# Kernel tuning notes

Measured on AMD Instinct MI355X. Metric: run time of the kernel, lower is better.

## Reference

```python
import jax, jax.numpy as jnp
import numpy as np

LN_EPS = 1e-5  # torch F.layer_norm default

def _layer_norm(c):
    mu = jnp.mean(c, axis=-1, keepdims=True)
    var = jnp.mean((c - mu) ** 2, axis=-1, keepdims=True)
    return (c - mu) * jax.lax.rsqrt(var + LN_EPS)

def _ln_lstm_cell(x, h, c, wx, wh, b):
    # wx: (4, H, in)  used as x @ wx[g].T ; wh: (4, H, H) used as h @ wh[g] (NO transpose,
    # matching the original torch code which only transposes the input weight).
    # gate order: i, f, o, c_tilde
    pre = jnp.einsum('bi,ghi->gbh', x, wx) + jnp.einsum('bh,ghk->gbk', h, wh) + b[:, None, :]
    i = jax.nn.sigmoid(pre[0])
    f = jax.nn.sigmoid(pre[1])
    o = jax.nn.sigmoid(pre[2])
    c_tilde = jnp.tanh(pre[3])
    c_new = _layer_norm(f * c + i * c_tilde)
    h_new = o * jnp.tanh(c_new)
    return h_new, c_new

def setup_inputs() -> dict:
    key = jax.random.key(0)
    ks = jax.random.split(key, 8)
    BS, SEQ, OBS, H, LOGIT = 512, 64, 512, 1024, 1024
    w = lambda k, *s: jax.random.normal(k, s, jnp.float32) * 0.02
    return {
        'obs': jax.random.normal(ks[0], (BS, SEQ, OBS), jnp.float32),
        'fc1_w': w(ks[1], H, OBS),
        'fc1_b': jnp.zeros((H,), jnp.float32),
        'wx1': w(ks[2], 4, H, H),
        'wh1': w(ks[3], 4, H, H),
        'b1': jnp.zeros((4, H), jnp.float32),
        'wx2': w(ks[4], 4, H, H),
        'wh2': w(ks[5], 4, H, H),
        'b2': jnp.zeros((4, H), jnp.float32),
        'fc2_w': w(ks[6], LOGIT, H),
        'fc2_b': jnp.zeros((LOGIT,), jnp.float32),
    }

def reference(obs, fc1_w, fc1_b, wx1, wh1, b1, wx2, wh2, b2, fc2_w, fc2_b):
    # obs: (bs, seq, obs_shape)
    x = jnp.einsum('bso,ho->bsh', obs, fc1_w) + fc1_b  # fc1 over all timesteps
    bs, seq, H = x.shape
    z = jnp.zeros((bs, H), x.dtype)

    def step(carry, xt):
        h0, c0, h1, c1 = carry
        h0, c0 = _ln_lstm_cell(xt, h0, c0, wx1, wh1, b1)  # layer 1
        h1, c1 = _ln_lstm_cell(h0, h1, c1, wx2, wh2, b2)  # layer 2 (dropout = identity in eval)
        return (h0, c0, h1, c1), None

    (h0, c0, h1, c1), _ = jax.lax.scan(step, (z, z, z, z), jnp.swapaxes(x, 0, 1))
    logit = h1 @ fc2_w.T + fc2_b
    h_n = jnp.stack((h0, h1), axis=0)
    c_n = jnp.stack((c0, c1), axis=0)
    return logit, h_n, c_n
```

## Files before the change

### kernel.cpp

```cpp
#include <hip/hip_runtime.h>
#include <hip/hip_bf16.h>
#include <hip/hip_fp16.h>

using half_t = _Float16;
typedef __attribute__((ext_vector_type(8))) _Float16 f16x8;
typedef __attribute__((ext_vector_type(4))) _Float16 f16x4;
typedef __attribute__((ext_vector_type(4))) float f32x4;

#define LN_EPS 1e-5f

__device__ inline void gll16(const void* g, void* ldsbase) {
    __builtin_amdgcn_global_load_lds(
        (const __attribute__((address_space(1))) void*)g,
        (__attribute__((address_space(3))) void*)ldsbase, 16, 0, 0);
}

__device__ inline float block_sum(float v, float* sred) {
    #pragma unroll
    for (int off = 32; off; off >>= 1) v += __shfl_down(v, off, 64);
    __syncthreads();
    if ((threadIdx.x & 63) == 0) sred[threadIdx.x >> 6] = v;
    __syncthreads();
    return sred[0] + sred[1] + sred[2] + sred[3];
}

__device__ inline void cell_block(
    int b, const half_t* __restrict__ preA, const half_t* __restrict__ preB,
    const float* __restrict__ bias,
    float* __restrict__ cst, half_t* __restrict__ hs,
    float* __restrict__ hf, bool final_step)
{
    __shared__ float sred[4];
    const int t = threadIdx.x;
    const int hi = t * 4;
    const size_t pb = (size_t)b * 4096 + hi;
    const size_t cb = (size_t)b * 1024 + hi;

    float pre[4][4];
    #pragma unroll
    for (int g = 0; g < 4; ++g) {
        f16x4 a4 = *(const f16x4*)&preA[pb + g*1024];
        f16x4 v4 = *(const f16x4*)&preB[pb + g*1024];
        float4 bs = *(const float4*)&bias[g*1024 + hi];
        pre[g][0] = (float)a4[0] + (float)v4[0] + bs.x;
        pre[g][1] = (float)a4[1] + (float)v4[1] + bs.y;
        pre[g][2] = (float)a4[2] + (float)v4[2] + bs.z;
        pre[g][3] = (float)a4[3] + (float)v4[3] + bs.w;
    }
    float4 c4 = *(const float4*)&cst[cb];
    float co[4] = {c4.x, c4.y, c4.z, c4.w};

    float cn[4], og[4], s = 0.f;
    #pragma unroll
    for (int j = 0; j < 4; ++j) {
        float ig = 1.f / (1.f + expf(-pre[0][j]));
        float fg = 1.f / (1.f + expf(-pre[1][j]));
        og[j]    = 1.f / (1.f + expf(-pre[2][j]));
        float ct = tanhf(pre[3][j]);
        cn[j] = fg * co[j] + ig * ct;
        s += cn[j];
    }
    float mu  = block_sum(s, sred) * (1.f/1024.f);
    float vs = 0.f;
    #pragma unroll
    for (int j = 0; j < 4; ++j) { float d = cn[j] - mu; vs += d*d; }
    float var = block_sum(vs, sred) * (1.f/1024.f);
    float rs  = rsqrtf(var + LN_EPS);

    float4 cw, hw; f16x4 h16w;
    #pragma unroll
    for (int j = 0; j < 4; ++j) {
        float cv = (cn[j] - mu) * rs;
        float hv = og[j] * tanhf(cv);
        ((float*)&cw)[j] = cv;
        ((float*)&hw)[j] = hv;
        h16w[j] = (half_t)hv;
    }
    *(float4*)&cst[cb] = cw;
    *(f16x4*)&hs[cb]   = h16w;
    if (final_step) *(float4*)&hf[cb] = hw;
}

__global__ __launch_bounds__(256) void cells_kernel(
    const half_t* __restrict__ preA1_rd, const half_t* __restrict__ preB1,
    const half_t* __restrict__ preA2,    const half_t* __restrict__ preB2,
    const float* __restrict__ b1, const float* __restrict__ b2,
    float* __restrict__ c0, float* __restrict__ c1,
    half_t* __restrict__ h0s, half_t* __restrict__ h1s,
    float* __restrict__ h0f, float* __restrict__ h1f, int st)
{
    const int blk = blockIdx.x;
    if (blk < 512) {
        cell_block(blk, preA1_rd, preB1, b1, c0, h0s, h0f, st == 63);
    } else {
        if (st == 0) return;
        cell_block(blk - 512, preA2, preB2, b2, c1, h1s, h1f, false);
    }
}

__global__ __launch_bounds__(256) void cells_final(
    const half_t* __restrict__ preA2, const half_t* __restrict__ preB2,
    const float* __restrict__ b2,
    float* __restrict__ c1, half_t* __restrict__ h1s, float* __restrict__ h1f)
{
    cell_block(blockIdx.x, preA2, preB2, b2, c1, h1s, h1f, true);
}

__global__ __launch_bounds__(256, 2) void step_gemm4(
    const half_t* __restrict__ X,
    const half_t* __restrict__ wx1c, const half_t* __restrict__ wx2c,
    const half_t* __restrict__ wh1t, const half_t* __restrict__ wh2t,
    half_t* __restrict__ preA1_wr, half_t* __restrict__ preA2,
    half_t* __restrict__ preB1, half_t* __restrict__ preB2,
    const half_t* __restrict__ h0s, const half_t* __restrict__ h1s, int st)
{
    __shared__ __align__(16) unsigned char sA[2][16384];
    __shared__ __align__(16) unsigned char sB[2][16384];

    const int wg = blockIdx.x;
    const int ylo = wg & 7;
    int r = wg >> 3;
    const int x = r & 3; r >>= 2;
    const int z = r & 3; r >>= 2;
    const int y = ylo + 8 * r;

    if (z == 3 && st == 63) return;

    const half_t* A; const half_t* B; half_t* C; size_t lda;
    if (z == 0)      { A = h0s; lda = 1024; B = wx2c; C = preA2; }
    else if (z == 1) { A = h1s; lda = 1024; B = wh2t; C = preB2; }
    else if (z == 2) { A = h0s; lda = 1024; B = wh1t; C = preB1; }
    else { A = X + (size_t)(st+1) * 1024; lda = 65536; B = wx1c; C = preA1_wr; }

    const int t = threadIdx.x, l = t & 63, w = t >> 6;
    const int wr = (w >> 1) * 64, wc = (w & 1) * 64;
    const int rowbase = x * 128, colbase = y * 128;

    int srow[4], sch[4];
    #pragma unroll
    for (int i = 0; i < 4; ++i) {
        int s = (w*4 + i)*64 + l;
        srow[i] = s >> 3;
        sch[i]  = ((s & 7) ^ (srow[i] & 7)) * 8;
    }

    f32x4 acc[4][4];
    #pragma unroll
    for (int m = 0; m < 4; ++m)
        #pragma unroll
        for (int n = 0; n < 4; ++n) acc[m][n] = (f32x4)(0.f);

    auto stage = [&](int kt, int buf) {
        const int ko = kt * 64;
        #pragma unroll
        for (int i = 0; i < 4; ++i) {
            gll16(A + (size_t)(rowbase+srow[i])*lda + ko + sch[i], &sA[buf][(w*4+i)*1024]);
            gll16(B + (size_t)(colbase+srow[i])*1024 + ko + sch[i], &sB[buf][(w*4+i)*1024]);
        }
    };

    stage(0, 0);
    for (int kt = 0; kt < 16; ++kt) {
        const int buf = kt & 1;
        __syncthreads();
        if (kt + 1 < 16) stage(kt + 1, buf ^ 1);
        #pragma unroll
        for (int kk = 0; kk < 2; ++kk) {
            const int chunk = kk*4 + (l >> 4);
            f16x8 bfr[4];
            #pragma unroll
            for (int n = 0; n < 4; ++n) {
                int rowb = wc + n*16 + (l & 15);
                bfr[n] = *(const f16x8*)&sB[buf][rowb*128 + ((chunk ^ (rowb & 7)) << 4)];
            }
            #pragma unroll
            for (int m = 0; m < 4; ++m) {
                int rowa = wr + m*16 + (l & 15);
                f16x8 af = *(const f16x8*)&sA[buf][rowa*128 + ((chunk ^ (rowa & 7)) << 4)];
                #pragma unroll
                for (int n = 0; n < 4; ++n)
                    acc[m][n] = __builtin_amdgcn_mfma_f32_16x16x32_f16(af, bfr[n], acc[m][n], 0, 0, 0);
            }
        }
    }

    #pragma unroll
    for (int m = 0; m < 4; ++m) {
        int row0 = rowbase + wr + m*16 + (l >> 4)*4;
        #pragma unroll
        for (int n = 0; n < 4; ++n) {
            int col = colbase + wc + n*16 + (l & 15);
            #pragma unroll
            for (int r2 = 0; r2 < 4; ++r2)
                C[(size_t)(row0+r2)*4096 + col] = (half_t)acc[m][n][r2];
        }
    }
}

struct GArgs {
    const half_t* A; const half_t* B; const float* bias; void* C;
    int lda, ldb, K, ldc, outhalf;
};

__global__ __launch_bounds__(256) void gemm_ms(GArgs g0, GArgs g1, GArgs g2,
                                               int gx, int gy, int gz, int rowpin)
{
    const int d = blockIdx.x;
    int x, y, z;
    if (rowpin) {
        const int xlo = d & 7;
        int r = d >> 3;
        y = r % gy;  r /= gy;
        z = r % gz;
        x = xlo + 8 * (r / gz);
    } else {
        const int ylo = d & 7;
        int r = d >> 3;
        x = r % gx;  r /= gx;
        z = r % gz;
        y = ylo + 8 * (r / gz);
    }

    const GArgs g = (z == 0) ? g0 : (z == 1 ? g1 : g2);

    __shared__ __align__(16) unsigned char sA[2][16384];
    __shared__ __align__(16) unsigned char sB[2][16384];

    const int t  = threadIdx.x;
    const int l  = t & 63;
    const int w  = t >> 6;
    const int wr = (w >> 1) * 64;
    const int wc = (w & 1)  * 64;
    const int rowbase = x * 128;
    const int colbase = y * 128;

    f32x4 acc[4][4];
    #pragma unroll
    for (int m = 0; m < 4; ++m)
        #pragma unroll
        for (int n = 0; n < 4; ++n) acc[m][n] = (f32x4)(0.f);

    int srow[4], sch[4];
    #pragma unroll
    for (int i = 0; i < 4; ++i) {
        int s = (w*4 + i)*64 + l;
        srow[i] = s >> 3;
        sch[i]  = ((s & 7) ^ (srow[i] & 7)) * 8;
    }

    const int nkt = g.K >> 6;

    auto stage = [&](int kt, int buf) {
        const int ko = kt * 64;
        #pragma unroll
        for (int i = 0; i < 4; ++i) {
            gll16(g.A + (size_t)(rowbase+srow[i])*g.lda + ko + sch[i], &sA[buf][(w*4+i)*1024]);
            gll16(g.B + (size_t)(colbase+srow[i])*g.ldb + ko + sch[i], &sB[buf][(w*4+i)*1024]);
        }
    };

    stage(0, 0);
    for (int kt = 0; kt < nkt; ++kt) {
        const int buf = kt & 1;
        __syncthreads();
        if (kt + 1 < nkt) stage(kt + 1, buf ^ 1);
        #pragma unroll
        for (int kk = 0; kk < 2; ++kk) {
            const int chunk = kk*4 + (l >> 4);
            f16x8 bfr[4];
            #pragma unroll
            for (int n = 0; n < 4; ++n) {
                int rowb = wc + n*16 + (l & 15);
                bfr[n] = *(const f16x8*)&sB[buf][rowb*128 + ((chunk ^ (rowb & 7)) << 4)];
            }
            #pragma unroll
            for (int m = 0; m < 4; ++m) {
                int rowa = wr + m*16 + (l & 15);
                f16x8 af = *(const f16x8*)&sA[buf][rowa*128 + ((chunk ^ (rowa & 7)) << 4)];
                #pragma unroll
                for (int n = 0; n < 4; ++n)
                    acc[m][n] = __builtin_amdgcn_mfma_f32_16x16x32_f16(af, bfr[n], acc[m][n], 0, 0, 0);
            }
        }
    }

    #pragma unroll
    for (int m = 0; m < 4; ++m) {
        int row0 = rowbase + wr + m*16 + (l >> 4)*4;
        #pragma unroll
        for (int n = 0; n < 4; ++n) {
            int col = colbase + wc + n*16 + (l & 15);
            float bv = g.bias ? g.bias[col] : 0.f;
            #pragma unroll
            for (int r2 = 0; r2 < 4; ++r2) {
                float v = acc[m][n][r2] + bv;
                if (g.outhalf) ((half_t*)g.C)[(size_t)(row0+r2)*g.ldc + col] = (half_t)v;
                else           ((float*)g.C)[(size_t)(row0+r2)*g.ldc + col] = v;
            }
        }
    }
}

__global__ __launch_bounds__(256) void transpose_wh_cvt(
    const float* __restrict__ wh1, const float* __restrict__ wh2,
    half_t* __restrict__ o1, half_t* __restrict__ o2)
{
    __shared__ float tile[64][65];
    const int z = blockIdx.z;
    const float* src = (z < 4 ? wh1 : wh2) + (size_t)(z & 3) * 1024 * 1024;
    half_t*      dst = (z < 4 ? o1  : o2 ) + (size_t)(z & 3) * 1024 * 1024;
    const int kb = blockIdx.x * 64, nb = blockIdx.y * 64;
    const int t = threadIdx.x;
    #pragma unroll
    for (int i = 0; i < 16; ++i) {
        int idx = t + i*256, r = idx >> 6, c = idx & 63;
        tile[r][c] = src[(size_t)(kb + r)*1024 + nb + c];
    }
    __syncthreads();
    #pragma unroll
    for (int i = 0; i < 16; ++i) {
        int idx = t + i*256, r = idx >> 6, c = idx & 63;
        dst[(size_t)(nb + r)*1024 + kb + c] = (half_t)tile[c][r];
    }
}

__global__ __launch_bounds__(256) void cvt_f32_f16(
    const float* __restrict__ in, half_t* __restrict__ out, int n8)
{
    int i = blockIdx.x * 256 + threadIdx.x;
    if (i >= n8) return;
    float4 lo = ((const float4*)in)[2*i];
    float4 hi = ((const float4*)in)[2*i + 1];
    union { uint4 v; half_t h[8]; } r;
    r.h[0]=(half_t)lo.x; r.h[1]=(half_t)lo.y; r.h[2]=(half_t)lo.z; r.h[3]=(half_t)lo.w;
    r.h[4]=(half_t)hi.x; r.h[5]=(half_t)hi.y; r.h[6]=(half_t)hi.z; r.h[7]=(half_t)hi.w;
    ((uint4*)out)[i] = r.v;
}

__global__ __launch_bounds__(256) void pack_out(
    const float* __restrict__ h0, const float* __restrict__ h1,
    const float* __restrict__ c0, const float* __restrict__ c1, float* __restrict__ out)
{
    const int NSZ = 512 * 1024;
    int i = blockIdx.x * 256 + threadIdx.x;
    out[NSZ     + i] = h0[i];
    out[2*NSZ   + i] = h1[i];
    out[3*NSZ   + i] = c0[i];
    out[4*NSZ   + i] = c1[i];
}

extern "C" void kernel_launch(void* const* d_in, const int* in_sizes, int n_in,
                              void* d_out, int out_size, void* d_ws, size_t ws_size,
                              hipStream_t stream)
{
    const float* obs   = (const float*)d_in[0];
    const float* fc1_w = (const float*)d_in[1];
    const float* fc1_b = (const float*)d_in[2];
    const float* wx1   = (const float*)d_in[3];
    const float* wh1   = (const float*)d_in[4];
    const float* b1    = (const float*)d_in[5];
    const float* wx2   = (const float*)d_in[6];
    const float* wh2   = (const float*)d_in[7];
    const float* b2    = (const float*)d_in[8];
    const float* fc2_w = (const float*)d_in[9];
    const float* fc2_b = (const float*)d_in[10];
    float* out = (float*)d_out;

    char* ws = (char*)d_ws;
    size_t off = 0;
    auto carve = [&](size_t bytes) -> char* {
        char* p = ws + off; off += (bytes + 255) & ~(size_t)255; return p;
    };
    half_t* obs16 = (half_t*)carve((size_t)512*64*512*2);
    half_t* wx1c  = (half_t*)carve((size_t)4096*1024*2);
    half_t* wh1t  = (half_t*)carve((size_t)4096*1024*2);
    half_t* wx2c  = (half_t*)carve((size_t)4096*1024*2);
    half_t* wh2t  = (half_t*)carve((size_t)4096*1024*2);
    half_t* fc1c  = (half_t*)carve((size_t)1024*512*2);
    half_t* fc2c  = (half_t*)carve((size_t)1024*1024*2);
    half_t* preA1a= (half_t*)carve((size_t)512*4096*2);
    half_t* preA1b= (half_t*)carve((size_t)512*4096*2);
    half_t* preA2 = (half_t*)carve((size_t)512*4096*2);
    half_t* preB1 = (half_t*)carve((size_t)512*4096*2);
    half_t* preB2 = (half_t*)carve((size_t)512*4096*2);
    half_t* h0s   = (half_t*)carve((size_t)512*1024*2);
    half_t* h1s   = (half_t*)carve((size_t)512*1024*2);
    float*  h0f   = (float*) carve((size_t)512*1024*4);
    float*  h1f   = (float*) carve((size_t)512*1024*4);
    float*  c0    = (float*) carve((size_t)512*1024*4);
    float*  c1    = (float*) carve((size_t)512*1024*4);

    const size_t X_bytes = (size_t)512*64*1024*2;
    bool modeB = (off + X_bytes) <= ws_size;
    half_t* X = (half_t*)carve(modeB ? X_bytes : (size_t)512*1024*2);

    hipMemsetAsync(h1s, 0, (size_t)512*1024*2, stream);
    hipMemsetAsync(c0,  0, (size_t)512*1024*4, stream);
    hipMemsetAsync(c1,  0, (size_t)512*1024*4, stream);
    hipMemsetAsync(preB1, 0, (size_t)512*4096*2, stream);

    cvt_f32_f16<<<8192, 256, 0, stream>>>(obs,   obs16, 512*64*512/8);
    cvt_f32_f16<<<2048, 256, 0, stream>>>(wx1,   wx1c,  4*1024*1024/8);
    cvt_f32_f16<<<2048, 256, 0, stream>>>(wx2,   wx2c,  4*1024*1024/8);
    cvt_f32_f16<<<256,  256, 0, stream>>>(fc1_w, fc1c,  1024*512/8);
    cvt_f32_f16<<<512,  256, 0, stream>>>(fc2_w, fc2c,  1024*1024/8);
    transpose_wh_cvt<<<dim3(16,16,8), 256, 0, stream>>>(wh1, wh2, wh1t, wh2t);

    GArgs Z{};
    auto ga = [](const half_t* A, int lda, const half_t* B, int ldb, int K,
                 const float* bias, void* C, int ldc, int outhalf) {
        GArgs g; g.A=A; g.B=B; g.bias=bias; g.C=C;
        g.lda=lda; g.ldb=ldb; g.K=K; g.ldc=ldc; g.outhalf=outhalf; return g;
    };

    if (modeB) {
        gemm_ms<<<256*8, 256, 0, stream>>>(
            ga(obs16, 512, fc1c, 512, 512, fc1_b, X, 1024, 1), Z, Z, 256, 8, 1, 1);
        gemm_ms<<<4*32, 256, 0, stream>>>(
            ga(X, 65536, wx1c, 1024, 1024, nullptr, preA1a, 4096, 1), Z, Z, 4, 32, 1, 0);

        for (int st = 0; st < 64; ++st) {
            const half_t* preA1_rd = (st & 1) ? preA1b : preA1a;
            half_t*       preA1_wr = (st & 1) ? preA1a : preA1b;
            cells_kernel<<<1024, 256, 0, stream>>>(
                preA1_rd, preB1, preA2, preB2, b1, b2,
                c0, c1, h0s, h1s, h0f, h1f, st);
            step_gemm4<<<512, 256, 0, stream>>>(
                X, wx1c, wx2c, wh1t, wh2t,
                preA1_wr, preA2, preB1, preB2, h0s, h1s, st);
        }
        cells_final<<<512, 256, 0, stream>>>(preA2, preB2, b2, c1, h1s, h1f);
    } else {
        for (int st = 0; st < 64; ++st) {
            gemm_ms<<<4*8, 256, 0, stream>>>(
                ga(obs16 + (size_t)st*512, 64*512, fc1c, 512, 512, fc1_b, X, 1024, 1),
                Z, Z, 4, 8, 1, 0);
            gemm_ms<<<4*32*2, 256, 0, stream>>>(
                ga(X, 1024,   wx1c, 1024, 1024, nullptr, preA1a, 4096, 1),
                ga(h0s, 1024, wh1t, 1024, 1024, nullptr, preB1, 4096, 1), Z, 4, 32, 2, 0);
            cells_kernel<<<1024, 256, 0, stream>>>(
                preA1a, preB1, preA2, preB2, b1, b2,
                c0, c1, h0s, h1s, h0f, h1f, st);
            gemm_ms<<<4*32*2, 256, 0, stream>>>(
                ga(h0s, 1024, wx2c, 1024, 1024, nullptr, preA2, 4096, 1),
                ga(h1s, 1024, wh2t, 1024, 1024, nullptr, preB2, 4096, 1), Z, 4, 32, 2, 0);
        }
        cells_final<<<512, 256, 0, stream>>>(preA2, preB2, b2, c1, h1s, h1f);
    }

    gemm_ms<<<4*8, 256, 0, stream>>>(
        ga(h1s, 1024, fc2c, 1024, 1024, fc2_b, out, 1024, 0), Z, Z, 4, 8, 1, 0);
    pack_out<<<2048, 256, 0, stream>>>(h0f, h1f, c0, c1, out);
}
```

Before: 2.389 ms.

## Fold fc1 into layer-1 input weights to shrink per-step input GEMM

Precomputes W1x = wx1 · fc1_w (a 4096x512 fp16 matrix) and folds fc1_b through wx1 into an adjusted bias b1x. The per-step layer-1 input GEMM now reads obs directly with K=512 instead of the K=1024 fc1 output, and the full X intermediate plus the fc1 GEMM over all timesteps are removed. This halves K for one of the four per-step GEMMs and drops the X buffer and the double-buffered preA1. The fp16 product W1x and reassociated sums change rounding, and the z=3 blocks now finish earlier than the rest, which may leave the per-step grid imbalanced.

```diff
diff --git a/kernel.cpp b/kernel.cpp
--- a/kernel.cpp
+++ b/kernel.cpp
@@ -82,16 +82,16 @@
 }
 
 __global__ __launch_bounds__(256) void cells_kernel(
-    const half_t* __restrict__ preA1_rd, const half_t* __restrict__ preB1,
-    const half_t* __restrict__ preA2,    const half_t* __restrict__ preB2,
-    const float* __restrict__ b1, const float* __restrict__ b2,
+    const half_t* __restrict__ preA1, const half_t* __restrict__ preB1,
+    const half_t* __restrict__ preA2, const half_t* __restrict__ preB2,
+    const float* __restrict__ b1x, const float* __restrict__ b2,
     float* __restrict__ c0, float* __restrict__ c1,
     half_t* __restrict__ h0s, half_t* __restrict__ h1s,
     float* __restrict__ h0f, float* __restrict__ h1f, int st)
 {
     const int blk = blockIdx.x;
     if (blk < 512) {
-        cell_block(blk, preA1_rd, preB1, b1, c0, h0s, h0f, st == 63);
+        cell_block(blk, preA1, preB1, b1x, c0, h0s, h0f, st == 63);
     } else {
         if (st == 0) return;
         cell_block(blk - 512, preA2, preB2, b2, c1, h1s, h1f, false);
@@ -107,10 +107,10 @@
 }
 
 __global__ __launch_bounds__(256, 2) void step_gemm4(
-    const half_t* __restrict__ X,
-    const half_t* __restrict__ wx1c, const half_t* __restrict__ wx2c,
+    const half_t* __restrict__ obs16,
+    const half_t* __restrict__ W1x, const half_t* __restrict__ wx2c,
     const half_t* __restrict__ wh1t, const half_t* __restrict__ wh2t,
-    half_t* __restrict__ preA1_wr, half_t* __restrict__ preA2,
+    half_t* __restrict__ preA1, half_t* __restrict__ preA2,
     half_t* __restrict__ preB1, half_t* __restrict__ preB2,
     const half_t* __restrict__ h0s, const half_t* __restrict__ h1s, int st)
 {
@@ -126,11 +126,11 @@
 
     if (z == 3 && st == 63) return;
 
-    const half_t* A; const half_t* B; half_t* C; size_t lda;
-    if (z == 0)      { A = h0s; lda = 1024; B = wx2c; C = preA2; }
-    else if (z == 1) { A = h1s; lda = 1024; B = wh2t; C = preB2; }
-    else if (z == 2) { A = h0s; lda = 1024; B = wh1t; C = preB1; }
-    else { A = X + (size_t)(st+1) * 1024; lda = 65536; B = wx1c; C = preA1_wr; }
+    const half_t* A; const half_t* B; half_t* C; size_t lda, ldb; int nkt;
+    if (z == 0)      { A = h0s; lda = 1024; B = wx2c; ldb = 1024; C = preA2; nkt = 16; }
+    else if (z == 1) { A = h1s; lda = 1024; B = wh2t; ldb = 1024; C = preB2; nkt = 16; }
+    else if (z == 2) { A = h0s; lda = 1024; B = wh1t; ldb = 1024; C = preB1; nkt = 16; }
+    else { A = obs16 + (size_t)(st+1) * 512; lda = 32768; B = W1x; ldb = 512; C = preA1; nkt = 8; }
 
     const int t = threadIdx.x, l = t & 63, w = t >> 6;
     const int wr = (w >> 1) * 64, wc = (w & 1) * 64;
@@ -155,15 +155,15 @@
         #pragma unroll
         for (int i = 0; i < 4; ++i) {
             gll16(A + (size_t)(rowbase+srow[i])*lda + ko + sch[i], &sA[buf][(w*4+i)*1024]);
-            gll16(B + (size_t)(colbase+srow[i])*1024 + ko + sch[i], &sB[buf][(w*4+i)*1024]);
+            gll16(B + (size_t)(colbase+srow[i])*ldb + ko + sch[i], &sB[buf][(w*4+i)*1024]);
         }
     };
 
     stage(0, 0);
-    for (int kt = 0; kt < 16; ++kt) {
+    for (int kt = 0; kt < nkt; ++kt) {
         const int buf = kt & 1;
         __syncthreads();
-        if (kt + 1 < 16) stage(kt + 1, buf ^ 1);
+        if (kt + 1 < nkt) stage(kt + 1, buf ^ 1);
         #pragma unroll
         for (int kk = 0; kk < 2; ++kk) {
             const int chunk = kk*4 + (l >> 4);
@@ -324,6 +324,38 @@
     }
 }
 
+__global__ __launch_bounds__(256) void transpose_fc1(
+    const float* __restrict__ fc1_w, half_t* __restrict__ fc1t)
+{
+    __shared__ float tile[64][65];
+    const int hb = blockIdx.x * 64, ob = blockIdx.y * 64;
+    const int t = threadIdx.x;
+    #pragma unroll
+    for (int i = 0; i < 16; ++i) {
+        int idx = t + i*256, r = idx >> 6, c = idx & 63;
+        tile[r][c] = fc1_w[(size_t)(hb + r)*512 + ob + c];
+    }
+    __syncthreads();
+    #pragma unroll
+    for (int i = 0; i < 16; ++i) {
+        int idx = t + i*256, r = idx >> 6, c = idx & 63;
+        fc1t[(size_t)(ob + r)*1024 + hb + c] = (half_t)tile[c][r];
+    }
+}
+
+__global__ __launch_bounds__(256) void fold_b1(
+    const float* __restrict__ wx1, const float* __restrict__ fc1_b,
+    const float* __restrict__ b1, float* __restrict__ b1x)
+{
+    __shared__ float sred[4];
+    const int j = blockIdx.x, t = threadIdx.x;
+    float4 wv = *(const float4*)&wx1[(size_t)j*1024 + t*4];
+    float4 bv = *(const float4*)&fc1_b[t*4];
+    float s = wv.x*bv.x + wv.y*bv.y + wv.z*bv.z + wv.w*bv.w;
+    float tot = block_sum(s, sred);
+    if (t == 0) b1x[j] = b1[j] + tot;
+}
+
 __global__ __launch_bounds__(256) void cvt_f32_f16(
     const float* __restrict__ in, half_t* __restrict__ out, int n8)
 {
@@ -376,10 +408,11 @@
     half_t* wh1t  = (half_t*)carve((size_t)4096*1024*2);
     half_t* wx2c  = (half_t*)carve((size_t)4096*1024*2);
     half_t* wh2t  = (half_t*)carve((size_t)4096*1024*2);
-    half_t* fc1c  = (half_t*)carve((size_t)1024*512*2);
+    half_t* fc1t  = (half_t*)carve((size_t)512*1024*2);
+    half_t* W1x   = (half_t*)carve((size_t)4096*512*2);
     half_t* fc2c  = (half_t*)carve((size_t)1024*1024*2);
-    half_t* preA1a= (half_t*)carve((size_t)512*4096*2);
-    half_t* preA1b= (half_t*)carve((size_t)512*4096*2);
+    float*  b1x   = (float*) carve((size_t)4096*4);
+    half_t* preA1 = (half_t*)carve((size_t)512*4096*2);
     half_t* preA2 = (half_t*)carve((size_t)512*4096*2);
     half_t* preB1 = (half_t*)carve((size_t)512*4096*2);
     half_t* preB2 = (half_t*)carve((size_t)512*4096*2);
@@ -390,10 +423,6 @@
     float*  c0    = (float*) carve((size_t)512*1024*4);
     float*  c1    = (float*) carve((size_t)512*1024*4);
 
-    const size_t X_bytes = (size_t)512*64*1024*2;
-    bool modeB = (off + X_bytes) <= ws_size;
-    half_t* X = (half_t*)carve(modeB ? X_bytes : (size_t)512*1024*2);
-
     hipMemsetAsync(h1s, 0, (size_t)512*1024*2, stream);
     hipMemsetAsync(c0,  0, (size_t)512*1024*4, stream);
     hipMemsetAsync(c1,  0, (size_t)512*1024*4, stream);
@@ -402,9 +431,10 @@
     cvt_f32_f16<<<8192, 256, 0, stream>>>(obs,   obs16, 512*64*512/8);
     cvt_f32_f16<<<2048, 256, 0, stream>>>(wx1,   wx1c,  4*1024*1024/8);
     cvt_f32_f16<<<2048, 256, 0, stream>>>(wx2,   wx2c,  4*1024*1024/8);
-    cvt_f32_f16<<<256,  256, 0, stream>>>(fc1_w, fc1c,  1024*512/8);
     cvt_f32_f16<<<512,  256, 0, stream>>>(fc2_w, fc2c,  1024*1024/8);
     transpose_wh_cvt<<<dim3(16,16,8), 256, 0, stream>>>(wh1, wh2, wh1t, wh2t);
+    transpose_fc1<<<dim3(16,8), 256, 0, stream>>>(fc1_w, fc1t);
+    fold_b1<<<4096, 256, 0, stream>>>(wx1, fc1_b, b1, b1x);
 
     GArgs Z{};
     auto ga = [](const half_t* A, int lda, const half_t* B, int ldb, int K,
@@ -413,40 +443,20 @@
         g.lda=lda; g.ldb=ldb; g.K=K; g.ldc=ldc; g.outhalf=outhalf; return g;
     };
 
-    if (modeB) {
-        gemm_ms<<<256*8, 256, 0, stream>>>(
-            ga(obs16, 512, fc1c, 512, 512, fc1_b, X, 1024, 1), Z, Z, 256, 8, 1, 1);
-        gemm_ms<<<4*32, 256, 0, stream>>>(
-            ga(X, 65536, wx1c, 1024, 1024, nullptr, preA1a, 4096, 1), Z, Z, 4, 32, 1, 0);
-
-        for (int st = 0; st < 64; ++st) {
-            const half_t* preA1_rd = (st & 1) ? preA1b : preA1a;
-            half_t*       preA1_wr = (st & 1) ? preA1a : preA1b;
-            cells_kernel<<<1024, 256, 0, stream>>>(
-                preA1_rd, preB1, preA2, preB2, b1, b2,
-                c0, c1, h0s, h1s, h0f, h1f, st);
-            step_gemm4<<<512, 256, 0, stream>>>(
-                X, wx1c, wx2c, wh1t, wh2t,
-                preA1_wr, preA2, preB1, preB2, h0s, h1s, st);
-        }
-        cells_final<<<512, 256, 0, stream>>>(preA2, preB2, b2, c1, h1s, h1f);
-    } else {
-        for (int st = 0; st < 64; ++st) {
-            gemm_ms<<<4*8, 256, 0, stream>>>(
-                ga(obs16 + (size_t)st*512, 64*512, fc1c, 512, 512, fc1_b, X, 1024, 1),
-                Z, Z, 4, 8, 1, 0);
-            gemm_ms<<<4*32*2, 256, 0, stream>>>(
-                ga(X, 1024,   wx1c, 1024, 1024, nullptr, preA1a, 4096, 1),
-                ga(h0s, 1024, wh1t, 1024, 1024, nullptr, preB1, 4096, 1), Z, 4, 32, 2, 0);
-            cells_kernel<<<1024, 256, 0, stream>>>(
-                preA1a, preB1, preA2, preB2, b1, b2,
-                c0, c1, h0s, h1s, h0f, h1f, st);
-            gemm_ms<<<4*32*2, 256, 0, stream>>>(
-                ga(h0s, 1024, wx2c, 1024, 1024, nullptr, preA2, 4096, 1),
-                ga(h1s, 1024, wh2t, 1024, 1024, nullptr, preB2, 4096, 1), Z, 4, 32, 2, 0);
-        }
-        cells_final<<<512, 256, 0, stream>>>(preA2, preB2, b2, c1, h1s, h1f);
-    }
+    gemm_ms<<<128, 256, 0, stream>>>(
+        ga(wx1c, 1024, fc1t, 1024, 1024, nullptr, W1x, 512, 1), Z, Z, 32, 4, 1, 1);
+    gemm_ms<<<128, 256, 0, stream>>>(
+        ga(obs16, 32768, W1x, 512, 512, nullptr, preA1, 4096, 1), Z, Z, 4, 32, 1, 0);
+
+    for (int st = 0; st < 64; ++st) {
+        cells_kernel<<<1024, 256, 0, stream>>>(
+            preA1, preB1, preA2, preB2, b1x, b2,
+            c0, c1, h0s, h1s, h0f, h1f, st);
+        step_gemm4<<<512, 256, 0, stream>>>(
+            obs16, W1x, wx2c, wh1t, wh2t,
+            preA1, preA2, preB1, preB2, h0s, h1s, st);
+    }
+    cells_final<<<512, 256, 0, stream>>>(preA2, preB2, b2, c1, h1s, h1f);
 
     gemm_ms<<<4*8, 256, 0, stream>>>(
         ga(h1s, 1024, fc2c, 1024, 1024, fc2_b, out, 1024, 0), Z, Z, 4, 8, 1, 0);
```

Measured after the change: 2.255 ms. 1.06x faster.
